# Kernel tuning notes

Hardware: AMD Instinct MI355X
Metric: run time of the kernel (lower is better)

The kernel has to match this reference:

```python
import jax, jax.numpy as jnp
import numpy as np

D_MODEL = 1024
H = 16
HD = D_MODEL // H
K = 4
B = 4
S = 2048
EPS = 1e-6


def causal_dwconv_silu(x, w):
    # x: [B, S, C], w: [C, K] depthwise causal conv (torch conv1d with left pad K-1)
    Kw = w.shape[1]
    xp = jnp.pad(x, ((0, 0), (Kw - 1, 0), (0, 0)))
    s = x.shape[1]
    y = sum(xp[:, j:j + s, :] * w[:, j] for j in range(Kw))
    return jax.nn.silu(y)


def l2norm(x):
    n = jnp.linalg.norm(x, axis=-1, keepdims=True)
    return x / jnp.maximum(n, EPS)


def setup_inputs() -> dict:
    key = jax.random.key(0)
    ks = jax.random.split(key, 9)
    inp = {
        "hidden": jax.random.normal(ks[0], (B, S, D_MODEL), jnp.float32),
        "qkv_w": jax.random.normal(ks[1], (3 * D_MODEL, D_MODEL), jnp.float32) * 0.02,
        "ctrl_w": jax.random.normal(ks[2], (2 * H + D_MODEL, D_MODEL), jnp.float32) * 0.02,
        "ctrl_b": jnp.concatenate([
            jnp.full((H,), 1.5, jnp.float32),      # alpha bias
            jnp.full((H,), -2.0, jnp.float32),     # beta bias
            jnp.full((D_MODEL,), -1.5, jnp.float32),  # output gate bias
        ]),
        "convq_w": jax.random.normal(ks[3], (D_MODEL, K), jnp.float32) * 0.1,
        "convk_w": jax.random.normal(ks[4], (D_MODEL, K), jnp.float32) * 0.1,
        "convv_w": jax.random.normal(ks[5], (D_MODEL, K), jnp.float32) * 0.1,
        "norm_w": jnp.ones((HD,), jnp.float32),
        "out_w": jax.random.normal(ks[6], (D_MODEL, D_MODEL), jnp.float32) * 0.02,
        "out_b": jnp.zeros((D_MODEL,), jnp.float32),
    }
    return inp


def reference(hidden, qkv_w, ctrl_w, ctrl_b, convq_w, convk_w, convv_w, norm_w, out_w, out_b):
    b, s, d_model = hidden.shape
    h = (ctrl_w.shape[0] - d_model) // 2
    hd = d_model // h

    # projections
    qkv = hidden @ qkv_w.T                     # [B,S,3D]
    q_in, k_in, v_in = jnp.split(qkv, 3, axis=-1)
    ctrl = hidden @ ctrl_w.T + ctrl_b          # [B,S,2H+D]
    alpha_in = ctrl[..., :h]
    beta_in = ctrl[..., h:2 * h]
    gate_in = ctrl[..., 2 * h:]

    # causal depthwise conv + silu, reshape heads, normalize q/k
    queries = l2norm(causal_dwconv_silu(q_in, convq_w).reshape(b, s, h, hd))
    keys = l2norm(causal_dwconv_silu(k_in, convk_w).reshape(b, s, h, hd))
    values = causal_dwconv_silu(v_in, convv_w).reshape(b, s, h, hd)

    alpha = jax.nn.sigmoid(alpha_in) * 0.98 + 0.01   # [B,S,H]
    beta = jax.nn.sigmoid(beta_in)                    # [B,S,H]
    out_gate = jax.nn.sigmoid(gate_in)                # [B,S,D]

    # delta-rule scan over time
    def step(state, xs):
        q, k, v, a, be = xs  # q,k,v: [B,H,HD]; a,be: [B,H]
        a_ = a[..., None, None]
        b_ = be[..., None, None]
        old = jnp.einsum('bhvk,bhk->bhv', state, k)
        state = a_ * (state - b_ * jnp.einsum('bhv,bhk->bhvk', old, k)) \
                + b_ * jnp.einsum('bhv,bhk->bhvk', v, k)
        read = jnp.einsum('bhvk,bhk->bhv', state, q)
        return state, read

    init_state = jnp.zeros((b, h, hd, hd), hidden.dtype)
    xs = (
        jnp.moveaxis(queries, 1, 0),  # [S,B,H,HD]
        jnp.moveaxis(keys, 1, 0),
        jnp.moveaxis(values, 1, 0),
        jnp.moveaxis(alpha, 1, 0),    # [S,B,H]
        jnp.moveaxis(beta, 1, 0),
    )
    _, reads = jax.lax.scan(step, init_state, xs)   # [S,B,H,HD]
    reads = jnp.moveaxis(reads, 0, 1)               # [B,S,H,HD]

    # RMSNorm over head_dim (time-independent -> applied after scan)
    normed = reads * jax.lax.rsqrt(jnp.mean(reads * reads, axis=-1, keepdims=True) + EPS) * norm_w
    flat = normed.reshape(b, s, d_model)
    projected = flat @ out_w.T + out_b
    return out_gate * projected
```

## Files before the change

### kernel.cpp

```cpp
#include <hip/hip_runtime.h>

#define DM 1024
#define NH 16
#define HDIM 64
#define BATCH 4
#define SEQ 2048
#define NCTRL 1056
#define NTOT 4128
#define MROWS 8192

typedef __attribute__((ext_vector_type(4))) float f32x4;
typedef __attribute__((ext_vector_type(8))) __bf16 bf16x8;
typedef __attribute__((ext_vector_type(4))) __bf16 bf16x4;

#define GLL16(g, l) __builtin_amdgcn_global_load_lds(                          \
    (__attribute__((address_space(1))) const void*)(g),                        \
    (__attribute__((address_space(3))) void*)(l), 16, 0, 0)

#define MFMA16(a, b, c) __builtin_amdgcn_mfma_f32_16x16x32_bf16((a), (b), (c), 0, 0, 0)

__device__ __forceinline__ float sigmoidf_(float x) {
  return 1.0f / (1.0f + __expf(-x));
}

__global__ void cast_kernel(const float* __restrict__ in, __bf16* __restrict__ out, long n) {
  long i = ((long)blockIdx.x * blockDim.x + threadIdx.x) * 4;
  if (i < n) {
    f32x4 v = *(const f32x4*)(in + i);
    bf16x4 o;
#pragma unroll
    for (int j = 0; j < 4; ++j) o[j] = (__bf16)v[j];
    *(bf16x4*)(out + i) = o;
  }
}

template <int MODE>
__global__ __launch_bounds__(256, 2) void gemm_bt(
    const __bf16* __restrict__ A, const __bf16* __restrict__ Bm, int N,
    float* __restrict__ outF, __bf16* __restrict__ outB,
    const float* __restrict__ bias, const __bf16* __restrict__ gate,
    float* __restrict__ alp, float* __restrict__ bet,
    __bf16* __restrict__ preK, __bf16* __restrict__ preV) {
  __shared__ alignas(16) __bf16 Alds[128][32];
  __shared__ alignas(16) __bf16 Blds[128][32];
  const int t = threadIdx.x;
  const int wave = t >> 6, lane = t & 63;
  const int l16 = lane & 15, lq = lane >> 4;
  const int wr = wave >> 1, wc = wave & 1;
  const int m0 = blockIdx.x * 128, n0 = blockIdx.y * 128;

  f32x4 acc[4][4];
#pragma unroll
  for (int i = 0; i < 4; ++i)
#pragma unroll
    for (int j = 0; j < 4; ++j)
#pragma unroll
      for (int e = 0; e < 4; ++e) acc[i][j][e] = 0.0f;

  const int srow = t >> 2;
  const int scol = (t & 3) * 8;
  const __bf16* ga0 = A + (long)(m0 + srow) * DM + scol;
  const __bf16* ga1 = ga0 + (long)64 * DM;
  int nb0 = n0 + srow;      if (nb0 > N - 1) nb0 = N - 1;
  int nb1 = n0 + 64 + srow; if (nb1 > N - 1) nb1 = N - 1;
  const __bf16* gb0 = Bm + (long)nb0 * DM + scol;
  const __bf16* gb1 = Bm + (long)nb1 * DM + scol;
  char* lA = (char*)(&Alds[0][0]) + t * 16;
  char* lB = (char*)(&Blds[0][0]) + t * 16;

  for (int kt = 0; kt < DM; kt += 32) {
    GLL16(ga0, lA); GLL16(ga1, lA + 4096);
    GLL16(gb0, lB); GLL16(gb1, lB + 4096);
    ga0 += 32; ga1 += 32; gb0 += 32; gb1 += 32;
    __syncthreads();
    bf16x8 af[4], bfr[4];
#pragma unroll
    for (int i = 0; i < 4; ++i) {
      af[i]  = *(const bf16x8*)(&Alds[wr * 64 + i * 16 + l16][lq * 8]);
      bfr[i] = *(const bf16x8*)(&Blds[wc * 64 + i * 16 + l16][lq * 8]);
    }
#pragma unroll
    for (int mi = 0; mi < 4; ++mi)
#pragma unroll
      for (int ni = 0; ni < 4; ++ni)
        acc[mi][ni] = MFMA16(af[mi], bfr[ni], acc[mi][ni]);
    __syncthreads();
  }

#pragma unroll
  for (int mi = 0; mi < 4; ++mi) {
#pragma unroll
    for (int ni = 0; ni < 4; ++ni) {
      const int col = n0 + wc * 64 + ni * 16 + l16;
#pragma unroll
      for (int j = 0; j < 4; ++j) {
        const int row = m0 + wr * 64 + mi * 16 + lq * 4 + j;
        float v = acc[mi][ni][j];
        if (MODE == 1) {
          if (col < DM) {
            outB[(long)row * DM + col] = (__bf16)v;
          } else if (col < 2 * DM) {
            preK[(long)row * DM + (col - DM)] = (__bf16)v;
          } else if (col < 3 * DM) {
            preV[(long)row * DM + (col - 2 * DM)] = (__bf16)v;
          } else if (col < NTOT) {
            const int cc = col - 3 * DM;
            const float vb = v + bias[cc];
            if (cc < 16)      alp[(long)row * NH + cc] = sigmoidf_(vb) * 0.98f + 0.01f;
            else if (cc < 32) bet[(long)row * NH + (cc - 16)] = sigmoidf_(vb);
            else              outB[0] = outB[0],
                              ((__bf16*)gate)[(long)row * DM + (cc - 32)] = (__bf16)vb;
          }
        } else {
          const float g = sigmoidf_((float)gate[(long)row * DM + col]);
          outF[(long)row * DM + col] = g * (v + bias[col]);
        }
      }
    }
  }
}

__global__ void conv3_kernel(const __bf16* __restrict__ Xq, const __bf16* __restrict__ Xk,
                             const __bf16* __restrict__ Xv,
                             const float* __restrict__ wq, const float* __restrict__ wk,
                             const float* __restrict__ wv,
                             __bf16* __restrict__ oq, __bf16* __restrict__ ok,
                             __bf16* __restrict__ ov) {
  const int which = blockIdx.y;
  const __bf16* X = (which == 0) ? Xq : (which == 1) ? Xk : Xv;
  const float* w  = (which == 0) ? wq : (which == 1) ? wk : wv;
  __bf16* out     = (which == 0) ? oq : (which == 1) ? ok : ov;
  const bool NORM = (which < 2);

  const int b = blockIdx.x >> 8;
  const int s0 = (blockIdx.x & 255) * 8;
  const int t = threadIdx.x;
  const int d = t * 4;

  f32x4 wr[4];
#pragma unroll
  for (int i = 0; i < 4; ++i) wr[i] = *(const f32x4*)(w + (long)(d + i) * 4);

  f32x4 x[4];
#pragma unroll
  for (int j = 0; j < 3; ++j) {
    const int s = s0 - 3 + j;
    if (s >= 0) {
      bf16x4 r = *(const bf16x4*)(X + (long)(b * SEQ + s) * DM + d);
#pragma unroll
      for (int e = 0; e < 4; ++e) x[j][e] = (float)r[e];
    } else {
#pragma unroll
      for (int e = 0; e < 4; ++e) x[j][e] = 0.f;
    }
  }

  for (int si = 0; si < 8; ++si) {
    const int s = s0 + si;
    bf16x4 r = *(const bf16x4*)(X + (long)(b * SEQ + s) * DM + d);
#pragma unroll
    for (int e = 0; e < 4; ++e) x[3][e] = (float)r[e];

    float y[4];
#pragma unroll
    for (int i = 0; i < 4; ++i) {
      y[i] = x[0][i] * wr[i][0] + x[1][i] * wr[i][1] + x[2][i] * wr[i][2] + x[3][i] * wr[i][3];
      y[i] *= sigmoidf_(y[i]);
    }
    float sc = 1.0f;
    if (NORM) {
      float ss = y[0] * y[0] + y[1] * y[1] + y[2] * y[2] + y[3] * y[3];
      ss += __shfl_xor(ss, 1);
      ss += __shfl_xor(ss, 2);
      ss += __shfl_xor(ss, 4);
      ss += __shfl_xor(ss, 8);
      sc = 1.0f / fmaxf(sqrtf(ss), 1e-6f);
    }
    bf16x4 o;
#pragma unroll
    for (int i = 0; i < 4; ++i) o[i] = (__bf16)(y[i] * sc);
    *(bf16x4*)(out + (long)(b * SEQ + s) * DM + d) = o;

    x[0] = x[1]; x[1] = x[2]; x[2] = x[3];
  }
}

__device__ __forceinline__ void stage_tile64(const __bf16* __restrict__ g,
                                             __bf16* __restrict__ l, int t) {
#pragma unroll
  for (int r = 0; r < 2; ++r) {
    const int id = t + 256 * r;
    const int row = id >> 3, c8 = (id & 7) * 8;
    bf16x8 v = *(const bf16x8*)(g + (long)row * DM + c8);
    *(bf16x8*)(l + row * 72 + c8) = v;
  }
}

__device__ __forceinline__ void stage_scr(const __bf16* __restrict__ g,
                                          __bf16* __restrict__ l, int t) {
#pragma unroll
  for (int r = 0; r < 2; ++r) {
    const int id = t + 256 * r;
    const int row = id >> 3, c8 = (id & 7) * 8;
    bf16x8 v = *(const bf16x8*)(g + row * 64 + c8);
    *(bf16x8*)(l + row * 72 + c8) = v;
  }
}

#define OA_KB   0
#define OA_VB   9216
#define OA_GPB  18432
#define OA_UBH  27648
#define OA_UBL  46080
#define OA_GPD  64512
#define OA_RHS  68864
#define OA_AV   77312
#define OA_IAV  77568
#define OA_BV   77824
#define OA_TOT  78080

__global__ __launch_bounds__(256) void wy_local(
    const __bf16* __restrict__ kf, const __bf16* __restrict__ vf,
    const float* __restrict__ alp, const float* __restrict__ bet,
    __bf16* __restrict__ u0hi_g, __bf16* __restrict__ u0lo_g,
    __bf16* __restrict__ mmat_g, float* __restrict__ avs_g,
    __bf16* __restrict__ tt_g, __bf16* __restrict__ chi_g, __bf16* __restrict__ clo_g) {
  __shared__ alignas(16) char lds[OA_TOT];
  __bf16* Kb   = (__bf16*)(lds + OA_KB);
  __bf16* Vb   = (__bf16*)(lds + OA_VB);
  __bf16* Gpbf = (__bf16*)(lds + OA_GPB);
  float*  Gpd  = (float*)(lds + OA_GPD);
  __bf16* Ubh  = (__bf16*)(lds + OA_UBH);
  __bf16* Ubl  = (__bf16*)(lds + OA_UBL);
  float*  RHSa = (float*)(lds + OA_RHS);
  float*  Avl  = (float*)(lds + OA_AV);
  float*  iAvl = (float*)(lds + OA_IAV);
  float*  bvl  = (float*)(lds + OA_BV);
  __bf16* KTl  = (__bf16*)(lds + OA_VB);
  __bf16* Ktsh = (__bf16*)(lds + OA_GPB);
  __bf16* Ktsl = (__bf16*)(lds + OA_GPD);
  __bf16* ETl  = (__bf16*)(lds + OA_UBL);

  const int t = threadIdx.x;
  const int wave = t >> 6, lane = t & 63;
  const int l16 = lane & 15, lq = lane >> 4;
  const int bh = blockIdx.x >> 5, c = blockIdx.x & 31;
  const int b = bh >> 4, h = bh & 15;
  const long cb = (long)b * SEQ * DM + h * HDIM + (long)c * 64 * DM;
  const long idx = (long)blockIdx.x;

  stage_tile64(kf + cb, Kb, t);
  stage_tile64(vf + cb, Vb, t);
  if (t < 64) {
    const long sidx = ((long)b * SEQ + c * 64 + t) * NH + h;
    const float a = alp[sidx];
    const float be = bet[sidx];
    float la = log2f(a);
#pragma unroll
    for (int off = 1; off < 64; off <<= 1) {
      const float tmp = __shfl_up(la, off);
      if (t >= off) la += tmp;
    }
    const float A = exp2f(la);
    Avl[t] = A; iAvl[t] = 1.0f / A; bvl[t] = be;
  }
  {
    float* z = (float*)Ubh;
    for (int i = t; i < 9216; i += 256) z[i] = 0.f;
  }
  __syncthreads();

  {
    float iA4[4];
#pragma unroll
    for (int j = 0; j < 4; ++j) iA4[j] = iAvl[wave * 16 + lq * 4 + j];
    for (int ni = 0; ni < 4; ++ni) {
      const int tcol = ni * 16 + l16;
      f32x4 accG = {0.f, 0.f, 0.f, 0.f};
#pragma unroll
      for (int kk = 0; kk < 2; ++kk) {
        bf16x8 a  = *(const bf16x8*)(Kb + (wave * 16 + l16) * 72 + kk * 32 + lq * 8);
        bf16x8 bk = *(const bf16x8*)(Kb + tcol * 72 + kk * 32 + lq * 8);
        accG = MFMA16(a, bk, accG);
      }
#pragma unroll
      for (int j = 0; j < 4; ++j) {
        const int irow = wave * 16 + lq * 4 + j;
        const float vg = accG[j] * iA4[j];
        Gpbf[tcol * 72 + irow] = (irow < tcol) ? (__bf16)vg : (__bf16)0.f;
        if (wave == ni) Gpd[tcol * 17 + (irow & 15)] = (irow < tcol) ? vg : 0.f;
      }
    }
  }
  __syncthreads();

#pragma unroll
  for (int m = 0; m < 4; ++m) {
    if (m > 0) {
#pragma unroll
      for (int i2 = 0; i2 < 2; ++i2) {
        const int cb2 = wave * 2 + i2;
        f32x4 acc = {0.f, 0.f, 0.f, 0.f};
#pragma unroll
        for (int kk = 0; kk < 2; ++kk) {
          bf16x8 a   = *(const bf16x8*)(Gpbf + (m * 16 + l16) * 72 + kk * 32 + lq * 8);
          bf16x8 bh8 = *(const bf16x8*)(Ubh + (cb2 * 16 + l16) * 72 + kk * 32 + lq * 8);
          bf16x8 bl8 = *(const bf16x8*)(Ubl + (cb2 * 16 + l16) * 72 + kk * 32 + lq * 8);
          acc = MFMA16(a, bh8, acc);
          acc = MFMA16(a, bl8, acc);
        }
#pragma unroll
        for (int j = 0; j < 4; ++j)
          RHSa[(lq * 4 + j) * 132 + cb2 * 16 + l16] = acc[j];
      }
      __syncthreads();
    }
    if (wave < 2) {
      float ub[16];
#pragma unroll
      for (int tp = 0; tp < 16; ++tp) {
        const int tt = m * 16 + tp;
        float acc = (m > 0) ? RHSa[tp * 132 + wave * 64 + lane] : 0.f;
#pragma unroll
        for (int j = 0; j < tp; ++j) acc += Gpd[tt * 17 + j] * ub[j];
        float u;
        if (wave == 0) {
          u = bvl[tt] * ((float)Vb[tt * 72 + lane] - Avl[tt] * acc);
        } else {
          u = ((tt == lane) ? bvl[lane] * Avl[lane] : 0.f) - bvl[tt] * Avl[tt] * acc;
        }
        ub[tp] = u;
      }
      const int crow = wave * 64 + lane;
#pragma unroll
      for (int g4 = 0; g4 < 4; ++g4) {
        bf16x4 hi4, lo4;
#pragma unroll
        for (int e = 0; e < 4; ++e) {
          const float u = ub[g4 * 4 + e];
          const __bf16 hh = (__bf16)u;
          hi4[e] = hh; lo4[e] = (__bf16)(u - (float)hh);
        }
        *(bf16x4*)(Ubh + crow * 72 + m * 16 + g4 * 4) = hi4;
        *(bf16x4*)(Ubl + crow * 72 + m * 16 + g4 * 4) = lo4;
      }
    }
    __syncthreads();
  }

#pragma unroll
  for (int r = 0; r < 2; ++r) {
    const int id = t + 256 * r;
    const int row = id >> 3, c8 = (id & 7) * 8;
    *(bf16x8*)(u0hi_g + idx * 4096 + row * 64 + c8) = *(const bf16x8*)(Ubh + row * 72 + c8);
    *(bf16x8*)(u0lo_g + idx * 4096 + row * 64 + c8) = *(const bf16x8*)(Ubl + row * 72 + c8);
  }
  {
    const int jb = t & 3, trow = t >> 2;
#pragma unroll
    for (int e = 0; e < 16; ++e) {
      const int j = jb * 16 + e;
      const float val = (float)Ubh[(64 + j) * 72 + trow] + (float)Ubl[(64 + j) * 72 + trow];
      mmat_g[idx * 4096 + trow * 64 + j] = (__bf16)val;
    }
  }
  if (t < 64) avs_g[idx * 64 + t] = Avl[t];
  {
    const float Pv = Avl[63];
    const int k = t >> 2, j0 = (t & 3) * 16;
#pragma unroll
    for (int gg = 0; gg < 2; ++gg) {
      bf16x8 h8, l8, kt8;
#pragma unroll
      for (int e = 0; e < 8; ++e) {
        const int j = j0 + gg * 8 + e;
        const float kv = (float)Kb[j * 72 + k];
        const float val = kv * (Pv * iAvl[j]);
        const __bf16 hh = (__bf16)val;
        h8[e] = hh; l8[e] = (__bf16)(val - (float)hh);
        kt8[e] = (__bf16)kv;
      }
      *(bf16x8*)(Ktsh + k * 72 + j0 + gg * 8) = h8;
      *(bf16x8*)(Ktsl + k * 72 + j0 + gg * 8) = l8;
      *(bf16x8*)(KTl + k * 72 + j0 + gg * 8) = kt8;
    }
  }
  __syncthreads();

#pragma unroll
  for (int ni = 0; ni < 4; ++ni) {
    const int kcol = ni * 16 + l16;
    f32x4 acc = {0.f, 0.f, 0.f, 0.f};
#pragma unroll
    for (int kk = 0; kk < 2; ++kk) {
      bf16x8 ah  = *(const bf16x8*)(Ubh + (wave * 16 + l16) * 72 + kk * 32 + lq * 8);
      bf16x8 al  = *(const bf16x8*)(Ubl + (wave * 16 + l16) * 72 + kk * 32 + lq * 8);
      bf16x8 bh8 = *(const bf16x8*)(Ktsh + kcol * 72 + kk * 32 + lq * 8);
      bf16x8 bl8 = *(const bf16x8*)(Ktsl + kcol * 72 + kk * 32 + lq * 8);
      acc = MFMA16(ah, bh8, acc);
      acc = MFMA16(ah, bl8, acc);
      acc = MFMA16(al, bh8, acc);
    }
#pragma unroll
    for (int j = 0; j < 4; ++j) {
      const int vrow = wave * 16 + lq * 4 + j;
      const float cv = acc[j];
      const __bf16 hh = (__bf16)cv;
      chi_g[idx * 4096 + vrow * 64 + kcol] = hh;
      clo_g[idx * 4096 + vrow * 64 + kcol] = (__bf16)(cv - (float)hh);
    }
  }
  __syncthreads();

#pragma unroll
  for (int ni = 0; ni < 4; ++ni) {
    const int jcol = ni * 16 + l16;
    f32x4 acc = {0.f, 0.f, 0.f, 0.f};
#pragma unroll
    for (int kk = 0; kk < 2; ++kk) {
      bf16x8 a = *(const bf16x8*)(Ktsh + (wave * 16 + l16) * 72 + kk * 32 + lq * 8);
      bf16x8 b = *(const bf16x8*)(Ubh + (64 + jcol) * 72 + kk * 32 + lq * 8);
      acc = MFMA16(a, b, acc);
    }
#pragma unroll
    for (int j = 0; j < 4; ++j) {
      const int krow = wave * 16 + lq * 4 + j;
      ETl[krow * 72 + jcol] = (__bf16)acc[j];
    }
  }
  __syncthreads();

  {
    const float Pv2 = Avl[63];
#pragma unroll
    for (int ni = 0; ni < 4; ++ni) {
      const int mcol = ni * 16 + l16;
      f32x4 acc = {0.f, 0.f, 0.f, 0.f};
#pragma unroll
      for (int kk = 0; kk < 2; ++kk) {
        bf16x8 a = *(const bf16x8*)(ETl + (wave * 16 + l16) * 72 + kk * 32 + lq * 8);
        bf16x8 b = *(const bf16x8*)(KTl + mcol * 72 + kk * 32 + lq * 8);
        acc = MFMA16(a, b, acc);
      }
#pragma unroll
      for (int j = 0; j < 4; ++j) {
        const int krow = wave * 16 + lq * 4 + j;
        const float tv = ((krow == mcol) ? Pv2 : 0.f) - acc[j];
        tt_g[idx * 4096 + krow * 64 + mcol] = (__bf16)tv;
      }
    }
  }
}

#define OF_KB  0
#define OF_QB  9216
#define OF_SWH 18432
#define OF_SWL 27648
#define OF_B1  36864
#define OF_B2  46080
#define OF_B3  55296
#define OF_B4  64512
#define OF_AV  73728
#define OF_IAV 73984
#define OF_TOT 74240

__global__ __launch_bounds__(256) void wy_finish(
    const __bf16* __restrict__ qf, const __bf16* __restrict__ kf,
    const __bf16* __restrict__ chi_g, const __bf16* __restrict__ clo_g,
    const __bf16* __restrict__ tt_g,
    const __bf16* __restrict__ u0hi_g, const __bf16* __restrict__ u0lo_g,
    const __bf16* __restrict__ mmat_g, const float* __restrict__ avs_g,
    __bf16* __restrict__ reads) {
  __shared__ alignas(16) char lds[OF_TOT];
  __bf16* KB  = (__bf16*)(lds + OF_KB);
  __bf16* QB  = (__bf16*)(lds + OF_QB);
  __bf16* SWH = (__bf16*)(lds + OF_SWH);
  __bf16* SWL = (__bf16*)(lds + OF_SWL);
  __bf16* B1  = (__bf16*)(lds + OF_B1);
  __bf16* B2  = (__bf16*)(lds + OF_B2);
  __bf16* B3  = (__bf16*)(lds + OF_B3);
  __bf16* B4  = (__bf16*)(lds + OF_B4);
  float*  AV  = (float*)(lds + OF_AV);
  float*  IAV = (float*)(lds + OF_IAV);

  const int t = threadIdx.x;
  const int wave = t >> 6, lane = t & 63;
  const int l16 = lane & 15, lq = lane >> 4;
  const int bh = blockIdx.x >> 5, c = blockIdx.x & 31;
  const int b = bh >> 4, h = bh & 15;
  const long cb = (long)b * SEQ * DM + h * HDIM + (long)c * 64 * DM;
  const long idx = (long)blockIdx.x;

  stage_tile64(kf + cb, KB, t);
  stage_tile64(qf + cb, QB, t);
  if (c >= 1) {
    stage_scr(chi_g + (idx - 1) * 4096, B1, t);
    stage_scr(clo_g + (idx - 1) * 4096, B2, t);
  }
  if (c >= 2) {
    stage_scr(chi_g + (idx - 2) * 4096, B3, t);
    stage_scr(tt_g + (idx - 1) * 4096, B4, t);
  }
  if (t < 64) {
    const float A = avs_g[idx * 64 + t];
    AV[t] = A; IAV[t] = 1.0f / A;
  }
  __syncthreads();

  {
    f32x4 s0[4];
#pragma unroll
    for (int ni = 0; ni < 4; ++ni) {
      const int tcol = ni * 16 + l16;
#pragma unroll
      for (int j = 0; j < 4; ++j) {
        const int vrow = wave * 16 + lq * 4 + j;
        s0[ni][j] = (c >= 1)
            ? ((float)B1[vrow * 72 + tcol] + (float)B2[vrow * 72 + tcol]) : 0.f;
      }
    }
    if (c >= 2) {
#pragma unroll
      for (int ni = 0; ni < 4; ++ni) {
        const int tcol = ni * 16 + l16;
#pragma unroll
        for (int kk = 0; kk < 2; ++kk) {
          bf16x8 a = *(const bf16x8*)(B3 + (wave * 16 + l16) * 72 + kk * 32 + lq * 8);
          bf16x8 b2 = *(const bf16x8*)(B4 + tcol * 72 + kk * 32 + lq * 8);
          s0[ni] = MFMA16(a, b2, s0[ni]);
        }
      }
    }
#pragma unroll
    for (int ni = 0; ni < 4; ++ni) {
      const int tcol = ni * 16 + l16;
#pragma unroll
      for (int j = 0; j < 4; ++j) {
        const int vrow = wave * 16 + lq * 4 + j;
        const float s = s0[ni][j];
        const __bf16 hh = (__bf16)s;
        SWH[vrow * 72 + tcol] = hh;
        SWL[vrow * 72 + tcol] = (__bf16)(s - (float)hh);
      }
    }
  }
  __syncthreads();

  stage_scr(u0hi_g + idx * 4096, B1, t);
  stage_scr(u0lo_g + idx * 4096, B2, t);
  stage_scr(mmat_g + idx * 4096, B3, t);
  {
    float iA4[4];
#pragma unroll
    for (int j = 0; j < 4; ++j) iA4[j] = IAV[wave * 16 + lq * 4 + j];
#pragma unroll
    for (int ni = 0; ni < 4; ++ni) {
      const int tcol = ni * 16 + l16;
      const float At = AV[tcol];
      f32x4 accQ = {0.f, 0.f, 0.f, 0.f};
#pragma unroll
      for (int kk = 0; kk < 2; ++kk) {
        bf16x8 a  = *(const bf16x8*)(KB + (wave * 16 + l16) * 72 + kk * 32 + lq * 8);
        bf16x8 bq = *(const bf16x8*)(QB + tcol * 72 + kk * 32 + lq * 8);
        accQ = MFMA16(a, bq, accQ);
      }
#pragma unroll
      for (int j = 0; j < 4; ++j) {
        const int irow = wave * 16 + lq * 4 + j;
        const float vq = accQ[j] * iA4[j] * At;
        B4[tcol * 72 + irow] = (irow <= tcol) ? (__bf16)vq : (__bf16)0.f;
      }
    }
  }
  __syncthreads();

  f32x4 accW[4], accWq[4];
#pragma unroll
  for (int ni = 0; ni < 4; ++ni) {
    const int tcol = ni * 16 + l16;
    f32x4 aW = {0.f, 0.f, 0.f, 0.f}, aQ = {0.f, 0.f, 0.f, 0.f};
#pragma unroll
    for (int pp = 0; pp < 2; ++pp) {
      const __bf16* Xp = pp ? SWL : SWH;
#pragma unroll
      for (int kk = 0; kk < 2; ++kk) {
        bf16x8 a  = *(const bf16x8*)(Xp + (wave * 16 + l16) * 72 + kk * 32 + lq * 8);
        bf16x8 bk = *(const bf16x8*)(KB + tcol * 72 + kk * 32 + lq * 8);
        bf16x8 bq = *(const bf16x8*)(QB + tcol * 72 + kk * 32 + lq * 8);
        aW = MFMA16(a, bk, aW);
        aQ = MFMA16(a, bq, aQ);
      }
    }
    accW[ni] = aW; accWq[ni] = aQ;
  }
#pragma unroll
  for (int ni = 0; ni < 4; ++ni) {
    const int tcol = ni * 16 + l16;
#pragma unroll
    for (int j = 0; j < 4; ++j) {
      const int vrow = wave * 16 + lq * 4 + j;
      const float w = accW[ni][j];
      const __bf16 hh = (__bf16)w;
      SWH[vrow * 72 + tcol] = hh;
      SWL[vrow * 72 + tcol] = (__bf16)(w - (float)hh);
    }
  }

  f32x4 uacc[4];
#pragma unroll
  for (int ni = 0; ni < 4; ++ni) {
    const int tcol = ni * 16 + l16;
    f32x4 acc = {0.f, 0.f, 0.f, 0.f};
#pragma unroll
    for (int pp = 0; pp < 2; ++pp) {
      const __bf16* Xp = pp ? SWL : SWH;
#pragma unroll
      for (int kk = 0; kk < 2; ++kk) {
        bf16x8 a  = *(const bf16x8*)(Xp + (wave * 16 + l16) * 72 + kk * 32 + lq * 8);
        bf16x8 bm = *(const bf16x8*)(B3 + tcol * 72 + kk * 32 + lq * 8);
        acc = MFMA16(a, bm, acc);
      }
    }
#pragma unroll
    for (int j = 0; j < 4; ++j) {
      const int vrow = wave * 16 + lq * 4 + j;
      uacc[ni][j] = (float)B1[vrow * 72 + tcol] + (float)B2[vrow * 72 + tcol] - acc[j];
    }
  }
#pragma unroll
  for (int ni = 0; ni < 4; ++ni) {
    const int tcol = ni * 16 + l16;
#pragma unroll
    for (int j = 0; j < 4; ++j) {
      const int vrow = wave * 16 + lq * 4 + j;
      const float u = uacc[ni][j];
      const __bf16 hh = (__bf16)u;
      B1[vrow * 72 + tcol] = hh;
      B2[vrow * 72 + tcol] = (__bf16)(u - (float)hh);
    }
  }

#pragma unroll
  for (int ni = 0; ni < 4; ++ni) {
    const int tcol = ni * 16 + l16;
    f32x4 acc = {0.f, 0.f, 0.f, 0.f};
#pragma unroll
    for (int pp = 0; pp < 2; ++pp) {
      const __bf16* Xp = pp ? B2 : B1;
#pragma unroll
      for (int kk = 0; kk < 2; ++kk) {
        bf16x8 a  = *(const bf16x8*)(Xp + (wave * 16 + l16) * 72 + kk * 32 + lq * 8);
        bf16x8 bq = *(const bf16x8*)(B4 + tcol * 72 + kk * 32 + lq * 8);
        acc = MFMA16(a, bq, acc);
      }
    }
    const float At = AV[tcol];
#pragma unroll
    for (int j = 0; j < 4; ++j) {
      const int vrow = wave * 16 + lq * 4 + j;
      const float r = At * accWq[ni][j] + acc[j];
      reads[cb + (long)tcol * DM + vrow] = (__bf16)r;
    }
  }
}

__global__ void rms_kernel(const __bf16* __restrict__ reads, const float* __restrict__ nw,
                           __bf16* __restrict__ out) {
  const long m = blockIdx.x;
  const int t = threadIdx.x;
  const int d = t * 4;
  bf16x4 rb = *(const bf16x4*)(reads + m * DM + d);
  f32x4 r;
#pragma unroll
  for (int i = 0; i < 4; ++i) r[i] = (float)rb[i];
  float ss = r[0] * r[0] + r[1] * r[1] + r[2] * r[2] + r[3] * r[3];
  ss += __shfl_xor(ss, 1);
  ss += __shfl_xor(ss, 2);
  ss += __shfl_xor(ss, 4);
  ss += __shfl_xor(ss, 8);
  const float sc = 1.0f / sqrtf(ss * (1.0f / HDIM) + 1e-6f);
  f32x4 w = *(const f32x4*)(nw + (t & 15) * 4);
  bf16x4 o;
#pragma unroll
  for (int i = 0; i < 4; ++i) o[i] = (__bf16)(r[i] * sc * w[i]);
  *(bf16x4*)(out + m * DM + d) = o;
}

extern "C" void kernel_launch(void* const* d_in, const int* in_sizes, int n_in,
                              void* d_out, int out_size, void* d_ws, size_t ws_size,
                              hipStream_t stream) {
  const float* hidden  = (const float*)d_in[0];
  const float* qkv_w   = (const float*)d_in[1];
  const float* ctrl_w  = (const float*)d_in[2];
  const float* ctrl_b  = (const float*)d_in[3];
  const float* convq_w = (const float*)d_in[4];
  const float* convk_w = (const float*)d_in[5];
  const float* convv_w = (const float*)d_in[6];
  const float* norm_w  = (const float*)d_in[7];
  const float* out_w   = (const float*)d_in[8];
  const float* out_b   = (const float*)d_in[9];
  float* out = (float*)d_out;

  char* ws = (char*)d_ws;
  size_t off = 0;
  auto alloc = [&](size_t bytes) -> void* {
    void* p = ws + off;
    off += (bytes + 255) & ~(size_t)255;
    return p;
  };
  const size_t MD2 = (size_t)MROWS * DM * 2;
  __bf16* w1_bf   = (__bf16*)alloc((size_t)NTOT * DM * 2);
  __bf16* hid_bf  = (__bf16*)alloc(MD2);
  __bf16* pre     = (__bf16*)alloc(MD2);
  __bf16* q_bf    = (__bf16*)alloc(MD2);
  __bf16* k_bf    = (__bf16*)alloc(MD2);
  __bf16* v_bf    = (__bf16*)alloc(MD2);
  __bf16* gate_bf = (__bf16*)alloc(MD2);
  float*  alp     = (float*)alloc((size_t)MROWS * NH * 4);
  float*  bet     = (float*)alloc((size_t)MROWS * NH * 4);
  __bf16* w2_bf   = (__bf16*)alloc((size_t)DM * DM * 2);
  __bf16* mmat_g  = (__bf16*)alloc((size_t)2048 * 4096 * 2);
  float*  avs_g   = (float*)alloc((size_t)2048 * 64 * 4);
  __bf16* reads_g = (__bf16*)alloc(MD2);
  __bf16* tt_g    = (__bf16*)alloc((size_t)2048 * 4096 * 2);
  __bf16* chi_g   = (__bf16*)alloc((size_t)2048 * 4096 * 2);
  __bf16* clo_g   = (__bf16*)alloc((size_t)2048 * 4096 * 2);
  __bf16* u0hi_g  = hid_bf;
  __bf16* u0lo_g  = pre;
  __bf16* preK    = tt_g;
  __bf16* preV    = chi_g;
  __bf16* normed  = hid_bf;

  cast_kernel<<<(MROWS * DM) / 1024, 256, 0, stream>>>(hidden, hid_bf, (long)MROWS * DM);
  cast_kernel<<<(3 * DM * DM) / 1024, 256, 0, stream>>>(qkv_w, w1_bf, (long)3 * DM * DM);
  cast_kernel<<<(NCTRL * DM) / 1024, 256, 0, stream>>>(ctrl_w, w1_bf + (long)3 * DM * DM, (long)NCTRL * DM);
  cast_kernel<<<(DM * DM) / 1024, 256, 0, stream>>>(out_w, w2_bf, (long)DM * DM);

  gemm_bt<1><<<dim3(MROWS / 128, (NTOT + 127) / 128), 256, 0, stream>>>(
      hid_bf, w1_bf, NTOT, nullptr, pre, ctrl_b, gate_bf, alp, bet, preK, preV);

  conv3_kernel<<<dim3(BATCH * (SEQ / 8), 3), 256, 0, stream>>>(
      pre, preK, preV, convq_w, convk_w, convv_w, q_bf, k_bf, v_bf);

  wy_local<<<BATCH * NH * 32, 256, 0, stream>>>(k_bf, v_bf, alp, bet,
                                                u0hi_g, u0lo_g, mmat_g, avs_g,
                                                tt_g, chi_g, clo_g);
  wy_finish<<<BATCH * NH * 32, 256, 0, stream>>>(q_bf, k_bf, chi_g, clo_g, tt_g,
                                                 u0hi_g, u0lo_g, mmat_g, avs_g, reads_g);

  rms_kernel<<<MROWS, 256, 0, stream>>>(reads_g, norm_w, normed);

  gemm_bt<2><<<dim3(MROWS / 128, DM / 128), 256, 0, stream>>>(
      normed, w2_bf, DM, out, nullptr, out_b, gate_bf, nullptr, nullptr, nullptr, nullptr);
}
```

Measured before the change: 317.1 us.

## Fuse RMSNorm into wy_finish and precompute block-inverse for local triangular solve

```diff
diff --git a/kernel.cpp b/kernel.cpp
--- a/kernel.cpp
+++ b/kernel.cpp
@@ -106,10 +106,13 @@
           } else if (col < NTOT) {
             const int cc = col - 3 * DM;
             const float vb = v + bias[cc];
-            if (cc < 16)      alp[(long)row * NH + cc] = sigmoidf_(vb) * 0.98f + 0.01f;
-            else if (cc < 32) bet[(long)row * NH + (cc - 16)] = sigmoidf_(vb);
-            else              outB[0] = outB[0],
-                              ((__bf16*)gate)[(long)row * DM + (cc - 32)] = (__bf16)vb;
+            if (cc < 16) {
+              alp[(long)row * NH + cc] = sigmoidf_(vb) * 0.98f + 0.01f;
+            } else if (cc < 32) {
+              bet[(long)row * NH + (cc - 16)] = sigmoidf_(vb);
+            } else {
+              ((__bf16*)gate)[(long)row * DM + (cc - 32)] = (__bf16)vb;
+            }
           }
         } else {
           const float g = sigmoidf_((float)gate[(long)row * DM + col]);
@@ -292,6 +295,29 @@
       }
     }
   }
+
+  {
+    const int m = wave;
+    const int cdi = lane & 15;
+    float bA16[16];
+#pragma unroll
+    for (int tp = 0; tp < 16; ++tp)
+      bA16[tp] = bvl[m * 16 + tp] * Avl[m * 16 + tp];
+    float dcol[16];
+#pragma unroll
+    for (int tp = 0; tp < 16; ++tp) {
+      float acc = (tp == cdi) ? 1.f : 0.f;
+#pragma unroll
+      for (int j = 0; j < 16; ++j)
+        if (j < tp) acc -= bA16[tp] * Gpd[(m * 16 + tp) * 17 + j] * dcol[j];
+      dcol[tp] = acc;
+    }
+    if (lane < 16) {
+#pragma unroll
+      for (int tp = 0; tp < 16; ++tp)
+        Gpd[(m * 16 + tp) * 17 + cdi] = dcol[tp];
+    }
+  }
   __syncthreads();
 
 #pragma unroll
@@ -316,19 +342,24 @@
       __syncthreads();
     }
     if (wave < 2) {
-      float ub[16];
+      const int col = wave * 64 + lane;
+      float rhs[16];
 #pragma unroll
       for (int tp = 0; tp < 16; ++tp) {
         const int tt = m * 16 + tp;
-        float acc = (m > 0) ? RHSa[tp * 132 + wave * 64 + lane] : 0.f;
-#pragma unroll
-        for (int j = 0; j < tp; ++j) acc += Gpd[tt * 17 + j] * ub[j];
-        float u;
-        if (wave == 0) {
-          u = bvl[tt] * ((float)Vb[tt * 72 + lane] - Avl[tt] * acc);
-        } else {
-          u = ((tt == lane) ? bvl[lane] * Avl[lane] : 0.f) - bvl[tt] * Avl[tt] * acc;
-        }
+        const float bA = bvl[tt] * Avl[tt];
+        const float R = (m > 0) ? RHSa[tp * 132 + col] : 0.f;
+        rhs[tp] = (wave == 0)
+            ? bvl[tt] * (float)Vb[tt * 72 + lane] - bA * R
+            : (((tt == lane) ? bA : 0.f) - bA * R);
+      }
+      float ub[16];
+#pragma unroll
+      for (int tp = 0; tp < 16; ++tp) {
+        float u = rhs[tp];
+#pragma unroll
+        for (int j = 0; j < 16; ++j)
+          if (j < tp) u += Gpd[(m * 16 + tp) * 17 + j] * rhs[j];
         ub[tp] = u;
       }
       const int crow = wave * 64 + lane;
@@ -419,8 +450,8 @@
 #pragma unroll
     for (int kk = 0; kk < 2; ++kk) {
       bf16x8 a = *(const bf16x8*)(Ktsh + (wave * 16 + l16) * 72 + kk * 32 + lq * 8);
-      bf16x8 b = *(const bf16x8*)(Ubh + (64 + jcol) * 72 + kk * 32 + lq * 8);
-      acc = MFMA16(a, b, acc);
+      bf16x8 b2 = *(const bf16x8*)(Ubh + (64 + jcol) * 72 + kk * 32 + lq * 8);
+      acc = MFMA16(a, b2, acc);
     }
 #pragma unroll
     for (int j = 0; j < 4; ++j) {
@@ -439,8 +470,8 @@
 #pragma unroll
       for (int kk = 0; kk < 2; ++kk) {
         bf16x8 a = *(const bf16x8*)(ETl + (wave * 16 + l16) * 72 + kk * 32 + lq * 8);
-        bf16x8 b = *(const bf16x8*)(KTl + mcol * 72 + kk * 32 + lq * 8);
-        acc = MFMA16(a, b, acc);
+        bf16x8 b2 = *(const bf16x8*)(KTl + mcol * 72 + kk * 32 + lq * 8);
+        acc = MFMA16(a, b2, acc);
       }
 #pragma unroll
       for (int j = 0; j < 4; ++j) {
@@ -462,7 +493,8 @@
 #define OF_B4  64512
 #define OF_AV  73728
 #define OF_IAV 73984
-#define OF_TOT 74240
+#define OF_RS  74240
+#define OF_TOT 75264
 
 __global__ __launch_bounds__(256) void wy_finish(
     const __bf16* __restrict__ qf, const __bf16* __restrict__ kf,
@@ -470,7 +502,7 @@
     const __bf16* __restrict__ tt_g,
     const __bf16* __restrict__ u0hi_g, const __bf16* __restrict__ u0lo_g,
     const __bf16* __restrict__ mmat_g, const float* __restrict__ avs_g,
-    __bf16* __restrict__ reads) {
+    const float* __restrict__ norm_w, __bf16* __restrict__ normed) {
   __shared__ alignas(16) char lds[OF_TOT];
   __bf16* KB  = (__bf16*)(lds + OF_KB);
   __bf16* QB  = (__bf16*)(lds + OF_QB);
@@ -482,6 +514,7 @@
   __bf16* B4  = (__bf16*)(lds + OF_B4);
   float*  AV  = (float*)(lds + OF_AV);
   float*  IAV = (float*)(lds + OF_IAV);
+  float*  RS  = (float*)(lds + OF_RS);
 
   const int t = threadIdx.x;
   const int wave = t >> 6, lane = t & 63;
@@ -639,7 +672,9 @@
       B2[vrow * 72 + tcol] = (__bf16)(u - (float)hh);
     }
   }
-
+  __syncthreads();
+
+  f32x4 rreg[4];
 #pragma unroll
   for (int ni = 0; ni < 4; ++ni) {
     const int tcol = ni * 16 + l16;
@@ -659,31 +694,44 @@
     for (int j = 0; j < 4; ++j) {
       const int vrow = wave * 16 + lq * 4 + j;
       const float r = At * accWq[ni][j] + acc[j];
-      reads[cb + (long)tcol * DM + vrow] = (__bf16)r;
-    }
-  }
-}
-
-__global__ void rms_kernel(const __bf16* __restrict__ reads, const float* __restrict__ nw,
-                           __bf16* __restrict__ out) {
-  const long m = blockIdx.x;
-  const int t = threadIdx.x;
-  const int d = t * 4;
-  bf16x4 rb = *(const bf16x4*)(reads + m * DM + d);
-  f32x4 r;
-#pragma unroll
-  for (int i = 0; i < 4; ++i) r[i] = (float)rb[i];
-  float ss = r[0] * r[0] + r[1] * r[1] + r[2] * r[2] + r[3] * r[3];
-  ss += __shfl_xor(ss, 1);
-  ss += __shfl_xor(ss, 2);
-  ss += __shfl_xor(ss, 4);
-  ss += __shfl_xor(ss, 8);
-  const float sc = 1.0f / sqrtf(ss * (1.0f / HDIM) + 1e-6f);
-  f32x4 w = *(const f32x4*)(nw + (t & 15) * 4);
-  bf16x4 o;
-#pragma unroll
-  for (int i = 0; i < 4; ++i) o[i] = (__bf16)(r[i] * sc * w[i]);
-  *(bf16x4*)(out + m * DM + d) = o;
+      rreg[ni][j] = r;
+      B3[vrow * 72 + tcol] = (__bf16)r;
+    }
+  }
+  __syncthreads();
+
+  {
+    const int colr = t & 63, qr = t >> 6;
+    float s = 0.f;
+#pragma unroll
+    for (int rr = 0; rr < 16; ++rr) {
+      const float x = (float)B3[(qr * 16 + rr) * 72 + colr];
+      s += x * x;
+    }
+    RS[qr * 64 + colr] = s;
+  }
+  __syncthreads();
+  if (t < 64) {
+    const float s = RS[t] + RS[64 + t] + RS[128 + t] + RS[192 + t];
+    RS[t] = 1.0f / sqrtf(s * (1.0f / HDIM) + 1e-6f);
+  }
+  __syncthreads();
+
+  {
+    float nw4[4];
+#pragma unroll
+    for (int j = 0; j < 4; ++j) nw4[j] = norm_w[wave * 16 + lq * 4 + j];
+#pragma unroll
+    for (int ni = 0; ni < 4; ++ni) {
+      const int tcol = ni * 16 + l16;
+      const float sc = RS[tcol];
+#pragma unroll
+      for (int j = 0; j < 4; ++j) {
+        const int vrow = wave * 16 + lq * 4 + j;
+        normed[cb + (long)tcol * DM + vrow] = (__bf16)(rreg[ni][j] * sc * nw4[j]);
+      }
+    }
+  }
 }
 
 extern "C" void kernel_launch(void* const* d_in, const int* in_sizes, int n_in,
@@ -721,7 +769,7 @@
   __bf16* w2_bf   = (__bf16*)alloc((size_t)DM * DM * 2);
   __bf16* mmat_g  = (__bf16*)alloc((size_t)2048 * 4096 * 2);
   float*  avs_g   = (float*)alloc((size_t)2048 * 64 * 4);
-  __bf16* reads_g = (__bf16*)alloc(MD2);
+  __bf16* normed_g= (__bf16*)alloc(MD2);
   __bf16* tt_g    = (__bf16*)alloc((size_t)2048 * 4096 * 2);
   __bf16* chi_g   = (__bf16*)alloc((size_t)2048 * 4096 * 2);
   __bf16* clo_g   = (__bf16*)alloc((size_t)2048 * 4096 * 2);
@@ -729,7 +777,6 @@
   __bf16* u0lo_g  = pre;
   __bf16* preK    = tt_g;
   __bf16* preV    = chi_g;
-  __bf16* normed  = hid_bf;
 
   cast_kernel<<<(MROWS * DM) / 1024, 256, 0, stream>>>(hidden, hid_bf, (long)MROWS * DM);
   cast_kernel<<<(3 * DM * DM) / 1024, 256, 0, stream>>>(qkv_w, w1_bf, (long)3 * DM * DM);
@@ -746,10 +793,9 @@
                                                 u0hi_g, u0lo_g, mmat_g, avs_g,
                                                 tt_g, chi_g, clo_g);
   wy_finish<<<BATCH * NH * 32, 256, 0, stream>>>(q_bf, k_bf, chi_g, clo_g, tt_g,
-                                                 u0hi_g, u0lo_g, mmat_g, avs_g, reads_g);
-
-  rms_kernel<<<MROWS, 256, 0, stream>>>(reads_g, norm_w, normed);
+                                                 u0hi_g, u0lo_g, mmat_g, avs_g,
+                                                 norm_w, normed_g);
 
   gemm_bt<2><<<dim3(MROWS / 128, DM / 128), 256, 0, stream>>>(
-      normed, w2_bf, DM, out, nullptr, out_b, gate_bf, nullptr, nullptr, nullptr, nullptr);
+      normed_g, w2_bf, DM, out, nullptr, out_b, gate_bf, nullptr, nullptr, nullptr, nullptr);
 }
```

After: 303.2 us. 4.4% less time.
